# Performance work log

Measured on AMD Instinct MI355X. Metric: run time of the kernel, lower is better.

The kernel has to match this reference:

```python
import jax, jax.numpy as jnp
import numpy as np

N_HEADS = 16
EMBED = 1024
HEAD_SIZE = 64
BLOCK = 2048
BATCH = 2
SEQ = 2048


def setup_inputs() -> dict:
    key = jax.random.key(0)
    ks = jax.random.split(key, 6)
    scale_e = 1.0 / np.sqrt(EMBED)
    x = jax.random.normal(ks[0], (BATCH, SEQ, EMBED), dtype=jnp.float32)
    # per-head Q/K/V projections (bias=False in nanoGPT-style SelfAttentionHead), stacked over heads
    wq = jax.random.normal(ks[1], (N_HEADS, EMBED, HEAD_SIZE), dtype=jnp.float32) * scale_e
    wk = jax.random.normal(ks[2], (N_HEADS, EMBED, HEAD_SIZE), dtype=jnp.float32) * scale_e
    wv = jax.random.normal(ks[3], (N_HEADS, EMBED, HEAD_SIZE), dtype=jnp.float32) * scale_e
    # output projection nn.Linear(embedding_size, embedding_size): y = x @ W^T + b
    w_proj = jax.random.normal(ks[4], (EMBED, EMBED), dtype=jnp.float32) * scale_e
    b_proj = jax.random.normal(ks[5], (EMBED,), dtype=jnp.float32) * 0.01
    return {"x": x, "wq": wq, "wk": wk, "wv": wv, "w_proj": w_proj, "b_proj": b_proj}


def reference(x, wq, wk, wv, w_proj, b_proj):
    B, S, E = x.shape
    # project all heads at once: [B, H, S, D]
    q = jnp.einsum('bse,hed->bhsd', x, wq)
    k = jnp.einsum('bse,hed->bhsd', x, wk)
    v = jnp.einsum('bse,hed->bhsd', x, wv)
    scale = 1.0 / jnp.sqrt(jnp.asarray(HEAD_SIZE, dtype=x.dtype))
    scores = jnp.einsum('bhqd,bhkd->bhqk', q, k) * scale  # [B,H,S,S]
    causal = jnp.tril(jnp.ones((S, S), dtype=bool))
    scores = jnp.where(causal, scores, -jnp.inf)
    attn = jax.nn.softmax(scores, axis=-1)  # (attn dropout inactive in eval)
    out = jnp.einsum('bhqk,bhkd->bhqd', attn, v)  # [B,H,S,D]
    # concat heads along last dim -> [B, S, H*D] == [B, S, E]
    out = out.transpose(0, 2, 1, 3).reshape(B, S, E)
    # output projection (dropout inactive in eval)
    return out @ w_proj.T + b_proj
```

## Files before the change

kernel.cpp:

```cpp
#include <hip/hip_runtime.h>
#include <hip/hip_bf16.h>


typedef __attribute__((ext_vector_type(4))) float  f32x4;
typedef __attribute__((ext_vector_type(8))) short  bf16x8;

#define S_LEN 2048
#define EMB   1024
#define NH    16
#define HD    64

#define LDSW 72

#define QSCALE 0.18033688011112042f

#if __has_builtin(__builtin_amdgcn_exp2f)
#define EXP2(x) __builtin_amdgcn_exp2f(x)
#else
#define EXP2(x) __exp2f(x)
#endif

__device__ __forceinline__ unsigned short f2bf(float f) {
    __hip_bfloat16 h = __float2bfloat16(f);
    return __builtin_bit_cast(unsigned short, h);
}
__device__ __forceinline__ unsigned int pk2bf(float a, float b) {
    unsigned int x = __builtin_bit_cast(unsigned int, a);
    unsigned int y = __builtin_bit_cast(unsigned int, b);
    x += 0x7FFFu + ((x >> 16) & 1u);
    y += 0x7FFFu + ((y >> 16) & 1u);
    return (x >> 16) | (y & 0xFFFF0000u);
}

__global__ __launch_bounds__(256) void prep(const float* __restrict__ x,
                                            const float* __restrict__ wq,
                                            const float* __restrict__ wk,
                                            const float* __restrict__ wv,
                                            const float* __restrict__ wproj,
                                            unsigned short* __restrict__ xb,
                                            unsigned short* __restrict__ wpb,
                                            unsigned short* __restrict__ wcat) {
    int blk = blockIdx.x;
    if (blk < 5120) {
        const float* in = (blk < 4096) ? x : wproj;
        unsigned short* out = (blk < 4096) ? xb : wpb;
        int bb = (blk < 4096) ? blk : blk - 4096;
        int i = (bb * 256 + threadIdx.x) * 4;
        float4 v = *(const float4*)(in + i);
        out[i + 0] = f2bf(v.x);
        out[i + 1] = f2bf(v.y);
        out[i + 2] = f2bf(v.z);
        out[i + 3] = f2bf(v.w);
    } else {
        int b2  = blk - 5120;
        int et  = b2 & 7;
        int h   = (b2 >> 3) & 15;
        int qkv = b2 >> 7;
        const float* w = (qkv == 0) ? wq : (qkv == 1) ? wk : wv;
        int t = threadIdx.x;
        int d = t & 63, es = t >> 6;
        int e0 = et * 128 + es * 32;

        unsigned short val[32];
        #pragma unroll
        for (int i = 0; i < 32; i++)
            val[i] = f2bf(w[(size_t)h * 65536 + (size_t)(e0 + i) * 64 + d]);

        size_t n = (size_t)qkv * 1024 + h * 64 + d;
        #pragma unroll
        for (int k = 0; k < 4; k++)
            *(uint4*)(wcat + n * 1024 + e0 + k * 8) = *(const uint4*)(val + k * 8);
    }
}

__device__ __forceinline__ void gemm_tile_core(const unsigned short* __restrict__ A,
                                               const unsigned short* __restrict__ Bt,
                                               int K, int m0, int n0,
                                               unsigned short* As, unsigned short* Bs,
                                               f32x4 acc[4][4]) {
    const int t    = threadIdx.x;
    const int wave = t >> 6, lane = t & 63;
    const int wm   = (wave >> 1) * 64, wn = (wave & 1) * 64;
    const int lr   = lane & 15, quad = lane >> 4;
    const int sr   = t >> 3;
    const int sc   = (t & 7) * 8;

    #pragma unroll
    for (int i = 0; i < 4; i++)
        #pragma unroll
        for (int j = 0; j < 4; j++) acc[i][j] = (f32x4)(0.0f);

    for (int k0 = 0; k0 < K; k0 += 64) {
        __syncthreads();
        #pragma unroll
        for (int p = 0; p < 4; ++p) {
            int r = p * 32 + sr;
            uint4 av = *(const uint4*)(A  + (size_t)(m0 + r) * K + k0 + sc);
            uint4 bv = *(const uint4*)(Bt + (size_t)(n0 + r) * K + k0 + sc);
            *(uint4*)(As + r * LDSW + sc) = av;
            *(uint4*)(Bs + r * LDSW + sc) = bv;
        }
        __syncthreads();
        #pragma unroll
        for (int kk = 0; kk < 64; kk += 32) {
            bf16x8 af[4], bfr[4];
            #pragma unroll
            for (int i = 0; i < 4; i++)
                af[i] = *(const bf16x8*)(As + (wm + i * 16 + lr) * LDSW + kk + quad * 8);
            #pragma unroll
            for (int j = 0; j < 4; j++)
                bfr[j] = *(const bf16x8*)(Bs + (wn + j * 16 + lr) * LDSW + kk + quad * 8);
            #pragma unroll
            for (int i = 0; i < 4; i++)
                #pragma unroll
                for (int j = 0; j < 4; j++)
                    acc[i][j] = __builtin_amdgcn_mfma_f32_16x16x32_bf16(af[i], bfr[j], acc[i][j], 0, 0, 0);
        }
    }
}

__global__ __launch_bounds__(256) void gemm_qkv(const unsigned short* __restrict__ xb,
                                                const unsigned short* __restrict__ wcat,
                                                unsigned short* __restrict__ qb,
                                                unsigned short* __restrict__ kb,
                                                unsigned short* __restrict__ vt) {
    __shared__ unsigned short Smem[2 * 128 * LDSW];
    unsigned short* As = Smem;
    unsigned short* Bs = Smem + 128 * LDSW;
    f32x4 acc[4][4];
    int m0 = blockIdx.x * 128, n0 = blockIdx.y * 128;
    gemm_tile_core(xb, wcat, EMB, m0, n0, As, Bs, acc);

    int t = threadIdx.x, wave = t >> 6, lane = t & 63;
    int wm = (wave >> 1) * 64, wn = (wave & 1) * 64, lr = lane & 15, quad = lane >> 4;
    int b  = m0 >> 11;
    int s0 = m0 & 2047;
    unsigned short* Tb = Smem;

    if (n0 < 2048) {
        bool isQ = (n0 < 1024);
        unsigned short* dst = isQ ? qb : kb;
        float sc = isQ ? QSCALE : 1.0f;
        __syncthreads();
        #pragma unroll
        for (int i = 0; i < 4; i++)
            #pragma unroll
            for (int j = 0; j < 4; j++)
                #pragma unroll
                for (int e = 0; e < 4; e++)
                    Tb[(wm + i * 16 + quad * 4 + e) * 136 + wn + j * 16 + lr] = f2bf(acc[i][j][e] * sc);
        __syncthreads();
        #pragma unroll
        for (int p = 0; p < 8; p++) {
            int r  = p * 16 + (t >> 4);
            int ch = (t & 15) * 8;
            int n  = n0 + ch;
            int h  = (n >> 6) & 15, d = ch & 63;
            *(uint4*)(dst + (((size_t)(b * NH + h)) * S_LEN + s0 + r) * HD + d) =
                *(const uint4*)(Tb + r * 136 + ch);
        }
    } else {
        __syncthreads();
        #pragma unroll
        for (int i = 0; i < 4; i++)
            #pragma unroll
            for (int j = 0; j < 4; j++)
                #pragma unroll
                for (int e = 0; e < 4; e++)
                    Tb[(wn + j * 16 + lr) * 136 + (wm + i * 16 + quad * 4 + e)] = f2bf(acc[i][j][e]);
        __syncthreads();
        #pragma unroll
        for (int p = 0; p < 8; p++) {
            int nl  = p * 16 + (t >> 4);
            int n   = n0 + nl;
            int h   = (n >> 6) & 15, d = n & 63;
            int col = (t & 15) * 8;
            *(uint4*)(vt + (((size_t)(b * NH + h)) * HD + d) * S_LEN + s0 + col) =
                *(const uint4*)(Tb + nl * 136 + col);
        }
    }
}

__global__ __launch_bounds__(256) void gemm_proj(const unsigned short* __restrict__ ao,
                                                 const unsigned short* __restrict__ wpb,
                                                 const float* __restrict__ bproj,
                                                 float* __restrict__ out) {
    __shared__ unsigned short Smem[2 * 128 * LDSW];
    f32x4 acc[4][4];
    int m0 = blockIdx.x * 128, n0 = blockIdx.y * 128;
    gemm_tile_core(ao, wpb, EMB, m0, n0, Smem, Smem + 128 * LDSW, acc);

    int t = threadIdx.x, wave = t >> 6, lane = t & 63;
    int wm = (wave >> 1) * 64, wn = (wave & 1) * 64, lr = lane & 15, quad = lane >> 4;
    #pragma unroll
    for (int i = 0; i < 4; i++)
        #pragma unroll
        for (int j = 0; j < 4; j++) {
            int n = n0 + wn + j * 16 + lr;
            float bias = bproj[n];
            #pragma unroll
            for (int e = 0; e < 4; e++) {
                int m = m0 + wm + i * 16 + quad * 4 + e;
                out[(size_t)m * EMB + n] = acc[i][j][e] + bias;
            }
        }
}

__global__ __launch_bounds__(512) void attn_mfma(const unsigned short* __restrict__ qb,
                                                 const unsigned short* __restrict__ kb,
                                                 const unsigned short* __restrict__ vtb,
                                                 unsigned short* __restrict__ ao) {
    __shared__ unsigned short Ks[2][64 * LDSW];
    __shared__ unsigned short Vs[2][64 * LDSW];
    __shared__ unsigned short Ps[128 * LDSW];

    int bIdx = blockIdx.x;
    int bh   = bIdx & 31;
    int grp  = bIdx >> 5;
    int chunk = (grp < 8) ? (15 - grp) : (grp - 8);
    int b = bh >> 4, h = bh & 15;
    int t = threadIdx.x, wave = t >> 6, lane = t & 63;
    int c = lane & 15, quad = lane >> 4;

    const unsigned short* Q  = qb  + (size_t)bh * S_LEN * HD;
    const unsigned short* K  = kb  + (size_t)bh * S_LEN * HD;
    const unsigned short* Vt = vtb + (size_t)bh * HD * S_LEN;

    int r0 = chunk * 128;
    int rw = r0 + wave * 16;

    bf16x8 Qf[2];
    #pragma unroll
    for (int ks = 0; ks < 2; ks++)
        Qf[ks] = *(const bf16x8*)(Q + (size_t)(rw + c) * HD + ks * 32 + quad * 8);

    f32x4 O[4];
    f32x4 lacc = (f32x4)(0.0f);
    #pragma unroll
    for (int dt = 0; dt < 4; dt++) O[dt] = (f32x4)(0.0f);

    const short oneb = (short)0x3F80;
    bf16x8 ones = {oneb, oneb, oneb, oneb, oneb, oneb, oneb, oneb};

    unsigned short* Pw = Ps + wave * 16 * LDSW;
    int sr = t >> 3, scg = (t & 7) * 8;

    int NT = (r0 + 128) >> 6;

    uint4 kpre = *(const uint4*)(K  + (size_t)sr * HD + scg);
    uint4 vpre = *(const uint4*)(Vt + (size_t)sr * S_LEN + scg);
    *(uint4*)(Ks[0] + sr * LDSW + scg) = kpre;
    *(uint4*)(Vs[0] + sr * LDSW + scg) = vpre;
    kpre = *(const uint4*)(K  + (size_t)(64 + sr) * HD + scg);
    vpre = *(const uint4*)(Vt + (size_t)sr * S_LEN + 64 + scg);

    for (int tt = 0; tt < NT; ++tt) {
        __syncthreads();
        if (tt + 1 < NT) {
            unsigned short* Kd = Ks[(tt + 1) & 1];
            unsigned short* Vd = Vs[(tt + 1) & 1];
            *(uint4*)(Kd + sr * LDSW + scg) = kpre;
            *(uint4*)(Vd + sr * LDSW + scg) = vpre;
            if (tt + 2 < NT) {
                kpre = *(const uint4*)(K  + (size_t)((tt + 2) * 64 + sr) * HD + scg);
                vpre = *(const uint4*)(Vt + (size_t)sr * S_LEN + (tt + 2) * 64 + scg);
            }
        }
        int j0 = tt << 6;
        if (j0 <= rw + 15) {
            const unsigned short* Kc = Ks[tt & 1];
            const unsigned short* Vc = Vs[tt & 1];

            f32x4 S4[4];
            #pragma unroll
            for (int kt = 0; kt < 4; kt++) S4[kt] = (f32x4)(0.0f);
            __builtin_amdgcn_s_setprio(1);
            #pragma unroll
            for (int ks = 0; ks < 2; ks++) {
                bf16x8 Kf[4];
                #pragma unroll
                for (int kt = 0; kt < 4; kt++)
                    Kf[kt] = *(const bf16x8*)(Kc + (kt * 16 + c) * LDSW + ks * 32 + quad * 8);
                #pragma unroll
                for (int kt = 0; kt < 4; kt++)
                    S4[kt] = __builtin_amdgcn_mfma_f32_16x16x32_bf16(Kf[kt], Qf[ks], S4[kt], 0, 0, 0);
            }
            __builtin_amdgcn_s_setprio(0);

            bool need_mask = (j0 + 63 > rw);
            #pragma unroll
            for (int kt = 0; kt < 4; kt++) {
                float p0 = EXP2(S4[kt][0]);
                float p1 = EXP2(S4[kt][1]);
                float p2 = EXP2(S4[kt][2]);
                float p3 = EXP2(S4[kt][3]);
                if (need_mask) {
                    int key  = j0 + kt * 16 + quad * 4;
                    int qrow = rw + c;
                    if (key + 0 > qrow) p0 = 0.0f;
                    if (key + 1 > qrow) p1 = 0.0f;
                    if (key + 2 > qrow) p2 = 0.0f;
                    if (key + 3 > qrow) p3 = 0.0f;
                }
                uint2 pk;
                pk.x = pk2bf(p0, p1);
                pk.y = pk2bf(p2, p3);
                *(uint2*)(Pw + c * LDSW + kt * 16 + quad * 4) = pk;
            }

            __builtin_amdgcn_s_setprio(1);
            #pragma unroll
            for (int ks = 0; ks < 2; ks++) {
                bf16x8 Af = *(const bf16x8*)(Pw + c * LDSW + ks * 32 + quad * 8);
                lacc = __builtin_amdgcn_mfma_f32_16x16x32_bf16(Af, ones, lacc, 0, 0, 0);
                #pragma unroll
                for (int dt = 0; dt < 4; dt++) {
                    bf16x8 Vf = *(const bf16x8*)(Vc + (dt * 16 + c) * LDSW + ks * 32 + quad * 8);
                    O[dt] = __builtin_amdgcn_mfma_f32_16x16x32_bf16(Af, Vf, O[dt], 0, 0, 0);
                }
            }
            __builtin_amdgcn_s_setprio(0);
        }
    }

    float inv[4];
    #pragma unroll
    for (int e = 0; e < 4; e++) inv[e] = 1.0f / lacc[e];

    #pragma unroll
    for (int dt = 0; dt < 4; dt++)
        #pragma unroll
        for (int e = 0; e < 4; e++)
            Ps[(wave * 16 + quad * 4 + e) * LDSW + dt * 16 + c] = f2bf(O[dt][e] * inv[e]);
    __syncthreads();
    #pragma unroll
    for (int p = 0; p < 2; p++) {
        int r = p * 64 + sr;
        *(uint4*)(ao + ((size_t)(b * S_LEN + r0 + r)) * EMB + h * HD + scg) =
            *(const uint4*)(Ps + r * LDSW + scg);
    }
}

extern "C" void kernel_launch(void* const* d_in, const int* in_sizes, int n_in,
                              void* d_out, int out_size, void* d_ws, size_t ws_size,
                              hipStream_t stream) {
    const float* x     = (const float*)d_in[0];
    const float* wq    = (const float*)d_in[1];
    const float* wk    = (const float*)d_in[2];
    const float* wv    = (const float*)d_in[3];
    const float* wproj = (const float*)d_in[4];
    const float* bproj = (const float*)d_in[5];
    float* out = (float*)d_out;

    char* ws = (char*)d_ws;
    unsigned short* xb   = (unsigned short*)(ws + 0);
    unsigned short* wcat = (unsigned short*)(ws + 8388608);
    unsigned short* wpb  = (unsigned short*)(ws + 14680064);
    unsigned short* qb   = (unsigned short*)(ws + 16777216);
    unsigned short* kb   = (unsigned short*)(ws + 25165824);
    unsigned short* vt   = (unsigned short*)(ws + 33554432);
    unsigned short* ao   = (unsigned short*)(ws + 41943040);

    prep<<<5504, 256, 0, stream>>>(x, wq, wk, wv, wproj, xb, wpb, wcat);
    gemm_qkv<<<dim3(32, 24), 256, 0, stream>>>(xb, wcat, qb, kb, vt);
    attn_mfma<<<512, 512, 0, stream>>>(qb, kb, vt, ao);
    gemm_proj<<<dim3(32, 8), 256, 0, stream>>>(ao, wpb, bproj, out);
}
```

Baseline: 180.1 us.

## Fuse fp32-to-bf16 conversion into GEMM loads and give attention waves 32 rows

The separate pass that converted x and w_proj to bf16 is removed. The GEMM tile loader now reads fp32 directly and packs it with v_cvt_pk_bf16_f32, which saves one full write and read of the activations through global memory. The attention kernel drops to 256 threads, with each wave handling two 16-row query groups so every K/V fragment loaded from LDS is reused twice. The trade-off is more registers per wave and fewer waves per block. The GEMMs' global loads are now fp32, twice the bytes per element, and get converted repeatedly across tiles.

```diff
diff --git a/kernel.cpp b/kernel.cpp
--- a/kernel.cpp
+++ b/kernel.cpp
@@ -24,57 +24,39 @@
     __hip_bfloat16 h = __float2bfloat16(f);
     return __builtin_bit_cast(unsigned short, h);
 }
-__device__ __forceinline__ unsigned int pk2bf(float a, float b) {
-    unsigned int x = __builtin_bit_cast(unsigned int, a);
-    unsigned int y = __builtin_bit_cast(unsigned int, b);
-    x += 0x7FFFu + ((x >> 16) & 1u);
-    y += 0x7FFFu + ((y >> 16) & 1u);
-    return (x >> 16) | (y & 0xFFFF0000u);
-}
-
-__global__ __launch_bounds__(256) void prep(const float* __restrict__ x,
-                                            const float* __restrict__ wq,
-                                            const float* __restrict__ wk,
-                                            const float* __restrict__ wv,
-                                            const float* __restrict__ wproj,
-                                            unsigned short* __restrict__ xb,
-                                            unsigned short* __restrict__ wpb,
-                                            unsigned short* __restrict__ wcat) {
+__device__ __forceinline__ unsigned int cvtpk(float lo, float hi) {
+    unsigned int r;
+    asm("v_cvt_pk_bf16_f32 %0, %1, %2" : "=v"(r) : "v"(lo), "v"(hi));
+    return r;
+}
+
+__global__ __launch_bounds__(256) void prep_wcat(const float* __restrict__ wq,
+                                                 const float* __restrict__ wk,
+                                                 const float* __restrict__ wv,
+                                                 unsigned short* __restrict__ wcat) {
     int blk = blockIdx.x;
-    if (blk < 5120) {
-        const float* in = (blk < 4096) ? x : wproj;
-        unsigned short* out = (blk < 4096) ? xb : wpb;
-        int bb = (blk < 4096) ? blk : blk - 4096;
-        int i = (bb * 256 + threadIdx.x) * 4;
-        float4 v = *(const float4*)(in + i);
-        out[i + 0] = f2bf(v.x);
-        out[i + 1] = f2bf(v.y);
-        out[i + 2] = f2bf(v.z);
-        out[i + 3] = f2bf(v.w);
-    } else {
-        int b2  = blk - 5120;
-        int et  = b2 & 7;
-        int h   = (b2 >> 3) & 15;
-        int qkv = b2 >> 7;
-        const float* w = (qkv == 0) ? wq : (qkv == 1) ? wk : wv;
-        int t = threadIdx.x;
-        int d = t & 63, es = t >> 6;
-        int e0 = et * 128 + es * 32;
-
-        unsigned short val[32];
-        #pragma unroll
-        for (int i = 0; i < 32; i++)
-            val[i] = f2bf(w[(size_t)h * 65536 + (size_t)(e0 + i) * 64 + d]);
-
-        size_t n = (size_t)qkv * 1024 + h * 64 + d;
-        #pragma unroll
-        for (int k = 0; k < 4; k++)
-            *(uint4*)(wcat + n * 1024 + e0 + k * 8) = *(const uint4*)(val + k * 8);
-    }
-}
-
-__device__ __forceinline__ void gemm_tile_core(const unsigned short* __restrict__ A,
-                                               const unsigned short* __restrict__ Bt,
+    int et  = blk & 7;
+    int h   = (blk >> 3) & 15;
+    int qkv = blk >> 7;
+    const float* w = (qkv == 0) ? wq : (qkv == 1) ? wk : wv;
+    int t = threadIdx.x;
+    int d = t & 63, es = t >> 6;
+    int e0 = et * 128 + es * 32;
+
+    unsigned short val[32];
+    #pragma unroll
+    for (int i = 0; i < 32; i++)
+        val[i] = f2bf(w[(size_t)h * 65536 + (size_t)(e0 + i) * 64 + d]);
+
+    size_t n = (size_t)qkv * 1024 + h * 64 + d;
+    #pragma unroll
+    for (int k = 0; k < 4; k++)
+        *(uint4*)(wcat + n * 1024 + e0 + k * 8) = *(const uint4*)(val + k * 8);
+}
+
+template<int AF32, int BF32>
+__device__ __forceinline__ void gemm_tile_core(const void* __restrict__ Av,
+                                               const void* __restrict__ Btv,
                                                int K, int m0, int n0,
                                                unsigned short* As, unsigned short* Bs,
                                                f32x4 acc[4][4]) {
@@ -95,8 +77,25 @@
         #pragma unroll
         for (int p = 0; p < 4; ++p) {
             int r = p * 32 + sr;
-            uint4 av = *(const uint4*)(A  + (size_t)(m0 + r) * K + k0 + sc);
-            uint4 bv = *(const uint4*)(Bt + (size_t)(n0 + r) * K + k0 + sc);
+            uint4 av, bv;
+            if (AF32) {
+                const float* Af = (const float*)Av + (size_t)(m0 + r) * K + k0 + sc;
+                float4 v0 = *(const float4*)Af;
+                float4 v1 = *(const float4*)(Af + 4);
+                av.x = cvtpk(v0.x, v0.y); av.y = cvtpk(v0.z, v0.w);
+                av.z = cvtpk(v1.x, v1.y); av.w = cvtpk(v1.z, v1.w);
+            } else {
+                av = *(const uint4*)((const unsigned short*)Av + (size_t)(m0 + r) * K + k0 + sc);
+            }
+            if (BF32) {
+                const float* Bf = (const float*)Btv + (size_t)(n0 + r) * K + k0 + sc;
+                float4 v0 = *(const float4*)Bf;
+                float4 v1 = *(const float4*)(Bf + 4);
+                bv.x = cvtpk(v0.x, v0.y); bv.y = cvtpk(v0.z, v0.w);
+                bv.z = cvtpk(v1.x, v1.y); bv.w = cvtpk(v1.z, v1.w);
+            } else {
+                bv = *(const uint4*)((const unsigned short*)Btv + (size_t)(n0 + r) * K + k0 + sc);
+            }
             *(uint4*)(As + r * LDSW + sc) = av;
             *(uint4*)(Bs + r * LDSW + sc) = bv;
         }
@@ -119,7 +118,7 @@
     }
 }
 
-__global__ __launch_bounds__(256) void gemm_qkv(const unsigned short* __restrict__ xb,
+__global__ __launch_bounds__(256) void gemm_qkv(const float* __restrict__ x,
                                                 const unsigned short* __restrict__ wcat,
                                                 unsigned short* __restrict__ qb,
                                                 unsigned short* __restrict__ kb,
@@ -129,7 +128,7 @@
     unsigned short* Bs = Smem + 128 * LDSW;
     f32x4 acc[4][4];
     int m0 = blockIdx.x * 128, n0 = blockIdx.y * 128;
-    gemm_tile_core(xb, wcat, EMB, m0, n0, As, Bs, acc);
+    gemm_tile_core<1, 0>(x, wcat, EMB, m0, n0, As, Bs, acc);
 
     int t = threadIdx.x, wave = t >> 6, lane = t & 63;
     int wm = (wave >> 1) * 64, wn = (wave & 1) * 64, lr = lane & 15, quad = lane >> 4;
@@ -182,13 +181,13 @@
 }
 
 __global__ __launch_bounds__(256) void gemm_proj(const unsigned short* __restrict__ ao,
-                                                 const unsigned short* __restrict__ wpb,
+                                                 const float* __restrict__ wproj,
                                                  const float* __restrict__ bproj,
                                                  float* __restrict__ out) {
     __shared__ unsigned short Smem[2 * 128 * LDSW];
     f32x4 acc[4][4];
     int m0 = blockIdx.x * 128, n0 = blockIdx.y * 128;
-    gemm_tile_core(ao, wpb, EMB, m0, n0, Smem, Smem + 128 * LDSW, acc);
+    gemm_tile_core<0, 1>(ao, wproj, EMB, m0, n0, Smem, Smem + 128 * LDSW, acc);
 
     int t = threadIdx.x, wave = t >> 6, lane = t & 63;
     int wm = (wave >> 1) * 64, wn = (wave & 1) * 64, lr = lane & 15, quad = lane >> 4;
@@ -206,7 +205,7 @@
         }
 }
 
-__global__ __launch_bounds__(512) void attn_mfma(const unsigned short* __restrict__ qb,
+__global__ __launch_bounds__(256) void attn_mfma(const unsigned short* __restrict__ qb,
                                                  const unsigned short* __restrict__ kb,
                                                  const unsigned short* __restrict__ vtb,
                                                  unsigned short* __restrict__ ao) {
@@ -227,53 +226,71 @@
     const unsigned short* Vt = vtb + (size_t)bh * HD * S_LEN;
 
     int r0 = chunk * 128;
-    int rw = r0 + wave * 16;
-
-    bf16x8 Qf[2];
-    #pragma unroll
-    for (int ks = 0; ks < 2; ks++)
-        Qf[ks] = *(const bf16x8*)(Q + (size_t)(rw + c) * HD + ks * 32 + quad * 8);
-
-    f32x4 O[4];
-    f32x4 lacc = (f32x4)(0.0f);
-    #pragma unroll
-    for (int dt = 0; dt < 4; dt++) O[dt] = (f32x4)(0.0f);
+    int rw = r0 + wave * 32;
+
+    bf16x8 Qf[2][2];
+    #pragma unroll
+    for (int g = 0; g < 2; g++)
+        #pragma unroll
+        for (int ks = 0; ks < 2; ks++)
+            Qf[g][ks] = *(const bf16x8*)(Q + (size_t)(rw + g * 16 + c) * HD + ks * 32 + quad * 8);
+
+    f32x4 O[2][4];
+    f32x4 lacc[2];
+    #pragma unroll
+    for (int g = 0; g < 2; g++) {
+        lacc[g] = (f32x4)(0.0f);
+        #pragma unroll
+        for (int dt = 0; dt < 4; dt++) O[g][dt] = (f32x4)(0.0f);
+    }
 
     const short oneb = (short)0x3F80;
     bf16x8 ones = {oneb, oneb, oneb, oneb, oneb, oneb, oneb, oneb};
 
-    unsigned short* Pw = Ps + wave * 16 * LDSW;
+    unsigned short* Pw = Ps + wave * 32 * LDSW;
     int sr = t >> 3, scg = (t & 7) * 8;
 
     int NT = (r0 + 128) >> 6;
 
-    uint4 kpre = *(const uint4*)(K  + (size_t)sr * HD + scg);
-    uint4 vpre = *(const uint4*)(Vt + (size_t)sr * S_LEN + scg);
-    *(uint4*)(Ks[0] + sr * LDSW + scg) = kpre;
-    *(uint4*)(Vs[0] + sr * LDSW + scg) = vpre;
-    kpre = *(const uint4*)(K  + (size_t)(64 + sr) * HD + scg);
-    vpre = *(const uint4*)(Vt + (size_t)sr * S_LEN + 64 + scg);
+    uint4 kpre0 = *(const uint4*)(K  + (size_t)sr * HD + scg);
+    uint4 kpre1 = *(const uint4*)(K  + (size_t)(sr + 32) * HD + scg);
+    uint4 vpre0 = *(const uint4*)(Vt + (size_t)sr * S_LEN + scg);
+    uint4 vpre1 = *(const uint4*)(Vt + (size_t)(sr + 32) * S_LEN + scg);
+    *(uint4*)(Ks[0] + sr * LDSW + scg)        = kpre0;
+    *(uint4*)(Ks[0] + (sr + 32) * LDSW + scg) = kpre1;
+    *(uint4*)(Vs[0] + sr * LDSW + scg)        = vpre0;
+    *(uint4*)(Vs[0] + (sr + 32) * LDSW + scg) = vpre1;
+    kpre0 = *(const uint4*)(K  + (size_t)(64 + sr) * HD + scg);
+    kpre1 = *(const uint4*)(K  + (size_t)(96 + sr) * HD + scg);
+    vpre0 = *(const uint4*)(Vt + (size_t)sr * S_LEN + 64 + scg);
+    vpre1 = *(const uint4*)(Vt + (size_t)(sr + 32) * S_LEN + 64 + scg);
 
     for (int tt = 0; tt < NT; ++tt) {
         __syncthreads();
         if (tt + 1 < NT) {
             unsigned short* Kd = Ks[(tt + 1) & 1];
             unsigned short* Vd = Vs[(tt + 1) & 1];
-            *(uint4*)(Kd + sr * LDSW + scg) = kpre;
-            *(uint4*)(Vd + sr * LDSW + scg) = vpre;
+            *(uint4*)(Kd + sr * LDSW + scg)        = kpre0;
+            *(uint4*)(Kd + (sr + 32) * LDSW + scg) = kpre1;
+            *(uint4*)(Vd + sr * LDSW + scg)        = vpre0;
+            *(uint4*)(Vd + (sr + 32) * LDSW + scg) = vpre1;
             if (tt + 2 < NT) {
-                kpre = *(const uint4*)(K  + (size_t)((tt + 2) * 64 + sr) * HD + scg);
-                vpre = *(const uint4*)(Vt + (size_t)sr * S_LEN + (tt + 2) * 64 + scg);
+                kpre0 = *(const uint4*)(K  + (size_t)((tt + 2) * 64 + sr) * HD + scg);
+                kpre1 = *(const uint4*)(K  + (size_t)((tt + 2) * 64 + 32 + sr) * HD + scg);
+                vpre0 = *(const uint4*)(Vt + (size_t)sr * S_LEN + (tt + 2) * 64 + scg);
+                vpre1 = *(const uint4*)(Vt + (size_t)(sr + 32) * S_LEN + (tt + 2) * 64 + scg);
             }
         }
         int j0 = tt << 6;
-        if (j0 <= rw + 15) {
+        if (j0 <= rw + 31) {
             const unsigned short* Kc = Ks[tt & 1];
             const unsigned short* Vc = Vs[tt & 1];
 
-            f32x4 S4[4];
-            #pragma unroll
-            for (int kt = 0; kt < 4; kt++) S4[kt] = (f32x4)(0.0f);
+            f32x4 S4[2][4];
+            #pragma unroll
+            for (int g = 0; g < 2; g++)
+                #pragma unroll
+                for (int kt = 0; kt < 4; kt++) S4[g][kt] = (f32x4)(0.0f);
             __builtin_amdgcn_s_setprio(1);
             #pragma unroll
             for (int ks = 0; ks < 2; ks++) {
@@ -283,59 +300,72 @@
                     Kf[kt] = *(const bf16x8*)(Kc + (kt * 16 + c) * LDSW + ks * 32 + quad * 8);
                 #pragma unroll
                 for (int kt = 0; kt < 4; kt++)
-                    S4[kt] = __builtin_amdgcn_mfma_f32_16x16x32_bf16(Kf[kt], Qf[ks], S4[kt], 0, 0, 0);
+                    S4[0][kt] = __builtin_amdgcn_mfma_f32_16x16x32_bf16(Kf[kt], Qf[0][ks], S4[0][kt], 0, 0, 0);
+                #pragma unroll
+                for (int kt = 0; kt < 4; kt++)
+                    S4[1][kt] = __builtin_amdgcn_mfma_f32_16x16x32_bf16(Kf[kt], Qf[1][ks], S4[1][kt], 0, 0, 0);
             }
             __builtin_amdgcn_s_setprio(0);
 
-            bool need_mask = (j0 + 63 > rw);
-            #pragma unroll
-            for (int kt = 0; kt < 4; kt++) {
-                float p0 = EXP2(S4[kt][0]);
-                float p1 = EXP2(S4[kt][1]);
-                float p2 = EXP2(S4[kt][2]);
-                float p3 = EXP2(S4[kt][3]);
-                if (need_mask) {
-                    int key  = j0 + kt * 16 + quad * 4;
-                    int qrow = rw + c;
-                    if (key + 0 > qrow) p0 = 0.0f;
-                    if (key + 1 > qrow) p1 = 0.0f;
-                    if (key + 2 > qrow) p2 = 0.0f;
-                    if (key + 3 > qrow) p3 = 0.0f;
+            #pragma unroll
+            for (int g = 0; g < 2; g++) {
+                bool need_mask = (j0 + 63 > rw + g * 16);
+                #pragma unroll
+                for (int kt = 0; kt < 4; kt++) {
+                    float p0 = EXP2(S4[g][kt][0]);
+                    float p1 = EXP2(S4[g][kt][1]);
+                    float p2 = EXP2(S4[g][kt][2]);
+                    float p3 = EXP2(S4[g][kt][3]);
+                    if (need_mask) {
+                        int key  = j0 + kt * 16 + quad * 4;
+                        int qrow = rw + g * 16 + c;
+                        if (key + 0 > qrow) p0 = 0.0f;
+                        if (key + 1 > qrow) p1 = 0.0f;
+                        if (key + 2 > qrow) p2 = 0.0f;
+                        if (key + 3 > qrow) p3 = 0.0f;
+                    }
+                    uint2 pk;
+                    pk.x = cvtpk(p0, p1);
+                    pk.y = cvtpk(p2, p3);
+                    *(uint2*)(Pw + (g * 16 + c) * LDSW + kt * 16 + quad * 4) = pk;
                 }
-                uint2 pk;
-                pk.x = pk2bf(p0, p1);
-                pk.y = pk2bf(p2, p3);
-                *(uint2*)(Pw + c * LDSW + kt * 16 + quad * 4) = pk;
             }
 
             __builtin_amdgcn_s_setprio(1);
             #pragma unroll
             for (int ks = 0; ks < 2; ks++) {
-                bf16x8 Af = *(const bf16x8*)(Pw + c * LDSW + ks * 32 + quad * 8);
-                lacc = __builtin_amdgcn_mfma_f32_16x16x32_bf16(Af, ones, lacc, 0, 0, 0);
+                bf16x8 Af0 = *(const bf16x8*)(Pw + c * LDSW + ks * 32 + quad * 8);
+                bf16x8 Af1 = *(const bf16x8*)(Pw + (16 + c) * LDSW + ks * 32 + quad * 8);
+                lacc[0] = __builtin_amdgcn_mfma_f32_16x16x32_bf16(Af0, ones, lacc[0], 0, 0, 0);
+                lacc[1] = __builtin_amdgcn_mfma_f32_16x16x32_bf16(Af1, ones, lacc[1], 0, 0, 0);
                 #pragma unroll
                 for (int dt = 0; dt < 4; dt++) {
                     bf16x8 Vf = *(const bf16x8*)(Vc + (dt * 16 + c) * LDSW + ks * 32 + quad * 8);
-                    O[dt] = __builtin_amdgcn_mfma_f32_16x16x32_bf16(Af, Vf, O[dt], 0, 0, 0);
+                    O[0][dt] = __builtin_amdgcn_mfma_f32_16x16x32_bf16(Af0, Vf, O[0][dt], 0, 0, 0);
+                    O[1][dt] = __builtin_amdgcn_mfma_f32_16x16x32_bf16(Af1, Vf, O[1][dt], 0, 0, 0);
                 }
             }
             __builtin_amdgcn_s_setprio(0);
         }
     }
 
-    float inv[4];
-    #pragma unroll
-    for (int e = 0; e < 4; e++) inv[e] = 1.0f / lacc[e];
-
-    #pragma unroll
-    for (int dt = 0; dt < 4; dt++)
-        #pragma unroll
-        for (int e = 0; e < 4; e++)
-            Ps[(wave * 16 + quad * 4 + e) * LDSW + dt * 16 + c] = f2bf(O[dt][e] * inv[e]);
+    float inv[2][4];
+    #pragma unroll
+    for (int g = 0; g < 2; g++)
+        #pragma unroll
+        for (int e = 0; e < 4; e++) inv[g][e] = 1.0f / lacc[g][e];
+
+    #pragma unroll
+    for (int g = 0; g < 2; g++)
+        #pragma unroll
+        for (int dt = 0; dt < 4; dt++)
+            #pragma unroll
+            for (int e = 0; e < 4; e++)
+                Ps[(wave * 32 + g * 16 + quad * 4 + e) * LDSW + dt * 16 + c] = f2bf(O[g][dt][e] * inv[g][e]);
     __syncthreads();
     #pragma unroll
-    for (int p = 0; p < 2; p++) {
-        int r = p * 64 + sr;
+    for (int p = 0; p < 4; p++) {
+        int r = p * 32 + sr;
         *(uint4*)(ao + ((size_t)(b * S_LEN + r0 + r)) * EMB + h * HD + scg) =
             *(const uint4*)(Ps + r * LDSW + scg);
     }
@@ -353,16 +383,14 @@
     float* out = (float*)d_out;
 
     char* ws = (char*)d_ws;
-    unsigned short* xb   = (unsigned short*)(ws + 0);
-    unsigned short* wcat = (unsigned short*)(ws + 8388608);
-    unsigned short* wpb  = (unsigned short*)(ws + 14680064);
-    unsigned short* qb   = (unsigned short*)(ws + 16777216);
-    unsigned short* kb   = (unsigned short*)(ws + 25165824);
-    unsigned short* vt   = (unsigned short*)(ws + 33554432);
-    unsigned short* ao   = (unsigned short*)(ws + 41943040);
-
-    prep<<<5504, 256, 0, stream>>>(x, wq, wk, wv, wproj, xb, wpb, wcat);
-    gemm_qkv<<<dim3(32, 24), 256, 0, stream>>>(xb, wcat, qb, kb, vt);
-    attn_mfma<<<512, 512, 0, stream>>>(qb, kb, vt, ao);
-    gemm_proj<<<dim3(32, 8), 256, 0, stream>>>(ao, wpb, bproj, out);
-}
+    unsigned short* wcat = (unsigned short*)(ws + 0);
+    unsigned short* qb   = (unsigned short*)(ws + 8388608);
+    unsigned short* kb   = (unsigned short*)(ws + 16777216);
+    unsigned short* vt   = (unsigned short*)(ws + 25165824);
+    unsigned short* ao   = (unsigned short*)(ws + 33554432);
+
+    prep_wcat<<<384, 256, 0, stream>>>(wq, wk, wv, wcat);
+    gemm_qkv<<<dim3(32, 24), 256, 0, stream>>>(x, wcat, qb, kb, vt);
+    attn_mfma<<<512, 256, 0, stream>>>(qb, kb, vt, ao);
+    gemm_proj<<<dim3(32, 8), 256, 0, stream>>>(ao, wproj, bproj, out);
+}
```

Measured after the change: 190.8 us. 5.9% more time.

## Use hardware bf16 pack conversion and smaller 64x128 tiles for output projection

Applied to the files above, without the earlier changes.

Replaces the software round-to-nearest bf16 packing with the v_cvt_pk_bf16_f32 instruction, in both the attention P conversion and the prep cast kernel. The prep cast kernel now also writes packed 8-byte stores instead of four scalar 2-byte stores. The output projection GEMM drops the shared 128x128 tile core for a dedicated 64x128 tile kernel, doubling the grid to 512 blocks to fill more CUs. The smaller tile lowers data reuse per block, and the new loop is single-buffered with a sync every k-step.

```diff
diff --git a/kernel.cpp b/kernel.cpp
--- a/kernel.cpp
+++ b/kernel.cpp
@@ -24,12 +24,10 @@
     __hip_bfloat16 h = __float2bfloat16(f);
     return __builtin_bit_cast(unsigned short, h);
 }
-__device__ __forceinline__ unsigned int pk2bf(float a, float b) {
-    unsigned int x = __builtin_bit_cast(unsigned int, a);
-    unsigned int y = __builtin_bit_cast(unsigned int, b);
-    x += 0x7FFFu + ((x >> 16) & 1u);
-    y += 0x7FFFu + ((y >> 16) & 1u);
-    return (x >> 16) | (y & 0xFFFF0000u);
+__device__ __forceinline__ unsigned int cvtpk(float lo, float hi) {
+    unsigned int r;
+    asm("v_cvt_pk_bf16_f32 %0, %1, %2" : "=v"(r) : "v"(lo), "v"(hi));
+    return r;
 }
 
 __global__ __launch_bounds__(256) void prep(const float* __restrict__ x,
@@ -47,10 +45,10 @@
         int bb = (blk < 4096) ? blk : blk - 4096;
         int i = (bb * 256 + threadIdx.x) * 4;
         float4 v = *(const float4*)(in + i);
-        out[i + 0] = f2bf(v.x);
-        out[i + 1] = f2bf(v.y);
-        out[i + 2] = f2bf(v.z);
-        out[i + 3] = f2bf(v.w);
+        uint2 pk;
+        pk.x = cvtpk(v.x, v.y);
+        pk.y = cvtpk(v.z, v.w);
+        *(uint2*)(out + i) = pk;
     } else {
         int b2  = blk - 5120;
         int et  = b2 & 7;
@@ -185,15 +183,59 @@
                                                  const unsigned short* __restrict__ wpb,
                                                  const float* __restrict__ bproj,
                                                  float* __restrict__ out) {
-    __shared__ unsigned short Smem[2 * 128 * LDSW];
-    f32x4 acc[4][4];
-    int m0 = blockIdx.x * 128, n0 = blockIdx.y * 128;
-    gemm_tile_core(ao, wpb, EMB, m0, n0, Smem, Smem + 128 * LDSW, acc);
-
-    int t = threadIdx.x, wave = t >> 6, lane = t & 63;
-    int wm = (wave >> 1) * 64, wn = (wave & 1) * 64, lr = lane & 15, quad = lane >> 4;
-    #pragma unroll
-    for (int i = 0; i < 4; i++)
+    __shared__ unsigned short Smem[(64 + 128) * LDSW];
+    unsigned short* As = Smem;
+    unsigned short* Bs = Smem + 64 * LDSW;
+    const int K = EMB;
+    int m0 = blockIdx.x * 64, n0 = blockIdx.y * 128;
+
+    const int t    = threadIdx.x;
+    const int wave = t >> 6, lane = t & 63;
+    const int wm   = (wave >> 1) * 32, wn = (wave & 1) * 64;
+    const int lr   = lane & 15, quad = lane >> 4;
+    const int sr   = t >> 3;
+    const int sc   = (t & 7) * 8;
+
+    f32x4 acc[2][4];
+    #pragma unroll
+    for (int i = 0; i < 2; i++)
+        #pragma unroll
+        for (int j = 0; j < 4; j++) acc[i][j] = (f32x4)(0.0f);
+
+    for (int k0 = 0; k0 < K; k0 += 64) {
+        __syncthreads();
+        #pragma unroll
+        for (int p = 0; p < 2; ++p) {
+            int r = p * 32 + sr;
+            uint4 av = *(const uint4*)(ao + (size_t)(m0 + r) * K + k0 + sc);
+            *(uint4*)(As + r * LDSW + sc) = av;
+        }
+        #pragma unroll
+        for (int p = 0; p < 4; ++p) {
+            int r = p * 32 + sr;
+            uint4 bv = *(const uint4*)(wpb + (size_t)(n0 + r) * K + k0 + sc);
+            *(uint4*)(Bs + r * LDSW + sc) = bv;
+        }
+        __syncthreads();
+        #pragma unroll
+        for (int kk = 0; kk < 64; kk += 32) {
+            bf16x8 af[2], bfr[4];
+            #pragma unroll
+            for (int i = 0; i < 2; i++)
+                af[i] = *(const bf16x8*)(As + (wm + i * 16 + lr) * LDSW + kk + quad * 8);
+            #pragma unroll
+            for (int j = 0; j < 4; j++)
+                bfr[j] = *(const bf16x8*)(Bs + (wn + j * 16 + lr) * LDSW + kk + quad * 8);
+            #pragma unroll
+            for (int i = 0; i < 2; i++)
+                #pragma unroll
+                for (int j = 0; j < 4; j++)
+                    acc[i][j] = __builtin_amdgcn_mfma_f32_16x16x32_bf16(af[i], bfr[j], acc[i][j], 0, 0, 0);
+        }
+    }
+
+    #pragma unroll
+    for (int i = 0; i < 2; i++)
         #pragma unroll
         for (int j = 0; j < 4; j++) {
             int n = n0 + wn + j * 16 + lr;
@@ -303,8 +345,8 @@
                     if (key + 3 > qrow) p3 = 0.0f;
                 }
                 uint2 pk;
-                pk.x = pk2bf(p0, p1);
-                pk.y = pk2bf(p2, p3);
+                pk.x = cvtpk(p0, p1);
+                pk.y = cvtpk(p2, p3);
                 *(uint2*)(Pw + c * LDSW + kt * 16 + quad * 4) = pk;
             }
 
@@ -364,5 +406,5 @@
     prep<<<5504, 256, 0, stream>>>(x, wq, wk, wv, wproj, xb, wpb, wcat);
     gemm_qkv<<<dim3(32, 24), 256, 0, stream>>>(xb, wcat, qb, kb, vt);
     attn_mfma<<<512, 512, 0, stream>>>(qb, kb, vt, ao);
-    gemm_proj<<<dim3(32, 8), 256, 0, stream>>>(ao, wpb, bproj, out);
-}
+    gemm_proj<<<dim3(64, 8), 256, 0, stream>>>(ao, wpb, bproj, out);
+}
```

Result: slower. 195.3 us (+8.5%).
